# Performance work log

Hardware: AMD Instinct MI355X
Metric: run time of the kernel (lower is better)

## Reference

```python
import jax, jax.numpy as jnp
import numpy as np

U, P, D, B, H = 8192, 4096, 64, 1024, 50
EPS = 1e-8  # torch.cosine_similarity eps


def setup_inputs() -> dict:
    key = jax.random.key(0)
    ks = jax.random.split(key, 11)
    inp = {}
    for i, name in enumerate(["A_up", "A_up_NR", "A_up_FR", "A_up_TR", "A_up_UR"]):
        inp[name] = jax.random.uniform(ks[i], (U, P), jnp.float32)
    inp["user_emb"] = jax.random.normal(ks[5], (U, D), jnp.float32) * 0.1
    inp["post_emb"] = jax.random.normal(ks[6], (P, D), jnp.float32) * 0.1
    inp["user_model"] = jax.random.normal(ks[7], (U, 4), jnp.float32)
    inp["X_source_id"] = jax.random.randint(ks[8], (B,), 0, P)
    inp["X_user_id"] = jax.random.randint(ks[9], (B,), 0, U)
    inp["X_rumer_id"] = jax.random.randint(ks[10], (B, H), 0, U)
    return inp


def _forward(A, user_emb, post_emb, W, X_source_id, X_rumer_id):
    # A: [5,U,P] stacked relations [base, NR, FR, TR, UR].
    # 2-layer LightGCN-style propagation, batched across all 5 relations:
    #   u_k = A @ p_{k-1};  p_k = A^T @ u_{k-1}
    u0, p0 = user_emb, post_emb
    u1 = jnp.einsum('rup,pd->rud', A, p0)    # [5,U,D]
    p1 = jnp.einsum('rup,ud->rpd', A, u0)    # [5,P,D]
    u2 = jnp.einsum('rup,rpd->rud', A, p1)
    p2 = jnp.einsum('rup,rud->rpd', A, u1)
    # fused stack+mean over the 3 layer outputs (x0, x1, x2)
    Xu = (u0[None] + u1 + u2) / 3.0          # [5,U,D]
    X_post_full = (p0 + p1[0] + p2[0]) / 3.0  # [P,D] (base relation only)

    base = Xu[0]   # [U,D]
    rel = Xu[1:]   # [4,U,D]

    # cosine similarity of base users vs each relation variant
    n0 = jnp.linalg.norm(base, axis=1)                # [U]
    nr = jnp.linalg.norm(rel, axis=2)                 # [4,U]
    sim = jnp.sum(base[None] * rel, axis=2) / jnp.maximum(n0[None] * nr, EPS)
    sim = sim.T                                       # [U,4]
    mask = (sim == sim.max(axis=1, keepdims=True)).astype(sim.dtype)
    simm = mask * sim
    var = jnp.log(jnp.std(simm, axis=1, ddof=1) + 1.0)  # [U]; torch.std is unbiased

    user = jnp.transpose(rel, (1, 0, 2))                 # [U,4,D]
    user_embedding = jnp.einsum('ua,uad->ud', W, user)   # [U,D]
    # note: post_embedding = A_pu @ user_embedding is computed in the original
    # get_Userembedding but never used by forward's outputs; omitted.

    X_post = X_post_full[X_source_id]                    # [B,D]
    Xvu = base[X_rumer_id]                               # [B,H,D]
    Xv = var[X_rumer_id]                                 # [B,H]
    X_var_user = jnp.einsum('bh,bhd->bd', Xv, Xvu)       # [B,D]
    AugUser = jnp.mean(user_embedding[X_rumer_id], axis=1)  # [B,D]
    X_mean_user = jnp.mean(Xvu, axis=1)                  # [B,D]
    return X_post, X_var_user, AugUser, X_mean_user


def reference(A_up, A_up_NR, A_up_FR, A_up_TR, A_up_UR,
              user_emb, post_emb, user_model,
              X_source_id, X_user_id, X_rumer_id):
    A = jnp.stack([A_up, A_up_NR, A_up_FR, A_up_TR, A_up_UR], axis=0)
    return _forward(A, user_emb, post_emb, user_model, X_source_id, X_rumer_id)
```

## Files before the change

kernel.cpp:

```cpp
#include <hip/hip_runtime.h>
#include <hip/hip_bf16.h>
#include <math.h>

#define U_DIM 8192
#define P_DIM 4096
#define B_DIM 1024
#define H_DIM 50
#define EPSV  1e-8f

typedef __attribute__((ext_vector_type(8))) short short8;
typedef __attribute__((ext_vector_type(4))) short short4v;
typedef __attribute__((ext_vector_type(2))) short short2v;
typedef __attribute__((ext_vector_type(4))) float f32x4;

#define AROW(m) ((m) * 40 + ((m) & ~7))

struct APtrs { const float* p[5]; };

__device__ inline unsigned short f2bf(float f) {
    unsigned int u = __float_as_uint(f);
    u += 0x7FFFu + ((u >> 16) & 1u);
    return (unsigned short)(u >> 16);
}

template<bool TRANS>
__global__ __launch_bounds__(256, 4) void gemm_n64(
    APtrs Aps, const float* Bmat, float* C,
    int K, int ldm, long strideB, long strideC, int kseg)
{
    const int tid  = threadIdx.x;
    const int wid  = tid >> 6;
    const int lane = tid & 63;
    const int m0   = blockIdx.x * 128;
    const float* Ag = Aps.p[blockIdx.y];
    const float* Bp = Bmat + (size_t)blockIdx.y * strideB;
    float*       Cp = C    + (size_t)blockIdx.y * strideC;
    const int k_begin = blockIdx.z * kseg;

    __shared__ __align__(16) unsigned short a_s[128 * 41];
    __shared__ __align__(16) unsigned short b_s[64 * 41];

    const float* ap;
    if (!TRANS) ap = Ag + (size_t)(m0 + (tid >> 1)) * K + k_begin + ((tid & 1) << 4);
    else        ap = Ag + (size_t)(k_begin + ((tid >> 5) << 2)) * ldm + m0 + ((tid & 31) << 2);
    const float* bp = Bp + ((size_t)(k_begin + ((tid >> 4) << 1)) << 6) + ((tid & 15) << 2);

    float4 ra[4], rb[2];
    if (!TRANS) {
#pragma unroll
        for (int j = 0; j < 4; ++j) ra[j] = ((const float4*)ap)[j];
    } else {
#pragma unroll
        for (int j = 0; j < 4; ++j) ra[j] = *(const float4*)(ap + (size_t)j * ldm);
    }
    rb[0] = *(const float4*)bp;
    rb[1] = *(const float4*)(bp + 64);

    f32x4 acc[2][4] = {};
    const int iters = kseg >> 5;

    for (int it = 0; it < iters; ++it) {
        if (!TRANS) {
            const int row = tid >> 1, ho = (tid & 1) << 4;
            const float* f = (const float*)ra;
            short8 w0, w1;
#pragma unroll
            for (int j = 0; j < 8; ++j) { w0[j] = (short)f2bf(f[j]); w1[j] = (short)f2bf(f[8 + j]); }
            unsigned short* d = a_s + AROW(row) + ho;
            *(short8*)d = w0;
            *(short8*)(d + 8) = w1;
        } else {
            const int bm = tid & 31, bk = tid >> 5;
            const float* f = (const float*)ra;
#pragma unroll
            for (int jm = 0; jm < 4; ++jm) {
                short4v w = { (short)f2bf(f[jm]),     (short)f2bf(f[4 + jm]),
                              (short)f2bf(f[8 + jm]), (short)f2bf(f[12 + jm]) };
                *(short4v*)(a_s + AROW((bm << 2) + jm) + (bk << 2)) = w;
            }
        }
        {
            const int bd = tid & 15, bk2 = tid >> 4;
            const float* f = (const float*)rb;
#pragma unroll
            for (int jd = 0; jd < 4; ++jd) {
                short2v w = { (short)f2bf(f[jd]), (short)f2bf(f[4 + jd]) };
                *(short2v*)(b_s + AROW((bd << 2) + jd) + (bk2 << 1)) = w;
            }
        }
        __syncthreads();

        if (it + 1 < iters) {
            if (!TRANS) {
                ap += 32;
#pragma unroll
                for (int j = 0; j < 4; ++j) ra[j] = ((const float4*)ap)[j];
            } else {
                ap += (size_t)32 * ldm;
#pragma unroll
                for (int j = 0; j < 4; ++j) ra[j] = *(const float4*)(ap + (size_t)j * ldm);
            }
            bp += 32 * 64;
            rb[0] = *(const float4*)bp;
            rb[1] = *(const float4*)(bp + 64);
        }

        const int ko   = (lane >> 4) << 3;
        const int mrow = (wid << 5) + (lane & 15);
        short8 af0 = *(const short8*)(a_s + AROW(mrow) + ko);
        short8 af1 = *(const short8*)(a_s + AROW(mrow + 16) + ko);
#pragma unroll
        for (int nt = 0; nt < 4; ++nt) {
            short8 bf = *(const short8*)(b_s + AROW((nt << 4) + (lane & 15)) + ko);
            acc[0][nt] = __builtin_amdgcn_mfma_f32_16x16x32_bf16(af0, bf, acc[0][nt], 0, 0, 0);
            acc[1][nt] = __builtin_amdgcn_mfma_f32_16x16x32_bf16(af1, bf, acc[1][nt], 0, 0, 0);
        }
        __syncthreads();
    }

    const int col   = lane & 15;
    const int rbase = (lane >> 4) << 2;
#pragma unroll
    for (int mt = 0; mt < 2; ++mt)
#pragma unroll
        for (int nt = 0; nt < 4; ++nt)
#pragma unroll
            for (int i = 0; i < 4; ++i) {
                int row = m0 + (wid << 5) + (mt << 4) + rbase + i;
                atomicAdd(&Cp[((size_t)row << 6) + (nt << 4) + col], acc[mt][nt][i]);
            }
}

__device__ inline float wsum(float v) {
#pragma unroll
    for (int off = 32; off > 0; off >>= 1) v += __shfl_xor(v, off, 64);
    return v;
}

__global__ __launch_bounds__(256) void user_stats_k(
    const float* __restrict__ u0, const float* __restrict__ u1,
    const float* __restrict__ u2, const float* __restrict__ W,
    float* __restrict__ base_o, float* __restrict__ var_o, float* __restrict__ ue_o)
{
    int u    = blockIdx.x * 4 + (threadIdx.x >> 6);
    int lane = threadIdx.x & 63;
    size_t ud = ((size_t)u << 6) + lane;

    float b0 = u0[ud];
    float xu[5];
#pragma unroll
    for (int r = 0; r < 5; ++r)
        xu[r] = (b0 + u1[(size_t)r * U_DIM * 64 + ud] + u2[(size_t)r * U_DIM * 64 + ud]) * (1.0f / 3.0f);

    float base = xu[0];
    float n0 = sqrtf(wsum(base * base));
    float sim[4];
#pragma unroll
    for (int a = 0; a < 4; ++a) {
        float d  = wsum(base * xu[a + 1]);
        float nr = sqrtf(wsum(xu[a + 1] * xu[a + 1]));
        sim[a] = d / fmaxf(n0 * nr, EPSV);
    }
    float smax = fmaxf(fmaxf(sim[0], sim[1]), fmaxf(sim[2], sim[3]));
    float ssum = 0.0f;
    float simm[4];
#pragma unroll
    for (int a = 0; a < 4; ++a) { simm[a] = (sim[a] == smax) ? sim[a] : 0.0f; ssum += simm[a]; }
    float mean = ssum * 0.25f;
    float vs = 0.0f;
#pragma unroll
    for (int a = 0; a < 4; ++a) { float t = simm[a] - mean; vs += t * t; }
    vs *= (1.0f / 3.0f);
    float var = logf(sqrtf(vs) + 1.0f);

    float ue = 0.0f;
#pragma unroll
    for (int a = 0; a < 4; ++a) ue += W[((size_t)u << 2) + a] * xu[a + 1];

    base_o[ud] = base;
    ue_o[ud]   = ue;
    if (lane == 0) var_o[u] = var;
}

__global__ __launch_bounds__(256) void gather_k(
    const float* __restrict__ p0, const float* __restrict__ p1r0, const float* __restrict__ p2,
    const float* __restrict__ base, const float* __restrict__ var, const float* __restrict__ ue,
    const int* __restrict__ src_id, const int* __restrict__ rumer, float* __restrict__ out)
{
    int b    = blockIdx.x * 4 + (threadIdx.x >> 6);
    int lane = threadIdx.x & 63;

    int sp = src_id[b];
    size_t spd = ((size_t)sp << 6) + lane;
    out[((size_t)b << 6) + lane] = (p0[spd] + p1r0[spd] + p2[spd]) * (1.0f / 3.0f);

    float xv = 0.0f, xm = 0.0f, au = 0.0f;
    for (int h = 0; h < H_DIM; ++h) {
        int uu = rumer[b * H_DIM + h];
        size_t uud = ((size_t)uu << 6) + lane;
        float bv = base[uud];
        xv += var[uu] * bv;
        xm += bv;
        au += ue[uud];
    }
    out[((size_t)(B_DIM     + b) << 6) + lane] = xv;
    out[((size_t)(2 * B_DIM + b) << 6) + lane] = au * (1.0f / H_DIM);
    out[((size_t)(3 * B_DIM + b) << 6) + lane] = xm * (1.0f / H_DIM);
}

extern "C" void kernel_launch(void* const* d_in, const int* in_sizes, int n_in,
                              void* d_out, int out_size, void* d_ws, size_t ws_size,
                              hipStream_t stream)
{
    const float* u0 = (const float*)d_in[5];
    const float* p0 = (const float*)d_in[6];
    const float* W  = (const float*)d_in[7];
    const int* src   = (const int*)d_in[8];
    const int* rumer = (const int*)d_in[10];
    float* out = (float*)d_out;

    APtrs Ap;
    for (int r = 0; r < 5; ++r) Ap.p[r] = (const float*)d_in[r];

    float* u1   = (float*)d_ws;
    float* p1   = u1 + 5l * U_DIM * 64;
    float* p2   = p1 + 5l * P_DIM * 64;
    float* u2   = p2 + (long)P_DIM * 64;
    float* base = u2 + 5l * U_DIM * 64;
    float* var  = base + (long)U_DIM * 64;
    float* ue   = var + U_DIM;

    size_t zero_bytes = (size_t)(5l * U_DIM * 64 + 5l * P_DIM * 64 + (long)P_DIM * 64 + 5l * U_DIM * 64) * sizeof(float);
    hipMemsetAsync(d_ws, 0, zero_bytes, stream);

    gemm_n64<false><<<dim3(64, 5, 4), 256, 0, stream>>>(Ap, p0, u1, P_DIM, 0, 0, (long)U_DIM * 64, 1024);
    gemm_n64<true ><<<dim3(32, 5, 8), 256, 0, stream>>>(Ap, u0, p1, U_DIM, P_DIM, 0, (long)P_DIM * 64, 1024);
    gemm_n64<false><<<dim3(64, 5, 4), 256, 0, stream>>>(Ap, p1, u2, P_DIM, 0, (long)P_DIM * 64, (long)U_DIM * 64, 1024);
    gemm_n64<true ><<<dim3(32, 1, 16), 256, 0, stream>>>(Ap, u1, p2, U_DIM, P_DIM, 0, 0, 512);

    user_stats_k<<<U_DIM / 4, 256, 0, stream>>>(u0, u1, u2, W, base, var, ue);
    gather_k<<<B_DIM / 4, 256, 0, stream>>>(p0, p1, p2, base, var, ue, src, rumer, out);
}
```

Measured before the change: 890.1 us.

## Pre-transpose dense operands to bf16 and stream GEMM fragments directly from global

Adds a transpose kernel that converts the small dense operands (p0, u0, p1, u1) into K-major bf16 buffers so each lane can load its MFMA B fragment directly. The GEMM drops LDS staging and both barriers, loads A fragments straight from global into registers with double-buffered prefetch, and converts them to bf16 in-register. The final transposed GEMM also gets a finer K split. The aim is to remove the LDS round trip and synchronisation overhead. In exchange it adds extra launches, and the transposed-A path uses scalar strided loads that may coalesce poorly.

```diff
diff --git a/kernel.cpp b/kernel.cpp
--- a/kernel.cpp
+++ b/kernel.cpp
@@ -1,5 +1,4 @@
 #include <hip/hip_runtime.h>
-#include <hip/hip_bf16.h>
 #include <math.h>
 
 #define U_DIM 8192
@@ -9,11 +8,7 @@
 #define EPSV  1e-8f
 
 typedef __attribute__((ext_vector_type(8))) short short8;
-typedef __attribute__((ext_vector_type(4))) short short4v;
-typedef __attribute__((ext_vector_type(2))) short short2v;
 typedef __attribute__((ext_vector_type(4))) float f32x4;
-
-#define AROW(m) ((m) * 40 + ((m) & ~7))
 
 struct APtrs { const float* p[5]; };
 
@@ -23,111 +18,121 @@
     return (unsigned short)(u >> 16);
 }
 
+__global__ __launch_bounds__(256) void transpose_bf16_k(
+    const float* __restrict__ in, unsigned short* __restrict__ out,
+    int K, long strideIn, long strideOut)
+{
+    __shared__ float t[64][65];
+    const int tid = threadIdx.x;
+    const int kb  = blockIdx.x * 64;
+    const float* ip = in + (size_t)blockIdx.y * strideIn + (size_t)kb * 64;
+#pragma unroll
+    for (int j = 0; j < 16; ++j) {
+        int idx = tid + j * 256;
+        t[idx >> 6][idx & 63] = ip[idx];
+    }
+    __syncthreads();
+    unsigned short* op = out + (size_t)blockIdx.y * strideOut;
+#pragma unroll
+    for (int j = 0; j < 16; ++j) {
+        int idx = tid + j * 256;
+        int d = idx >> 6, k = idx & 63;
+        op[(size_t)d * K + kb + k] = f2bf(t[k][d]);
+    }
+}
+
 template<bool TRANS>
 __global__ __launch_bounds__(256, 4) void gemm_n64(
-    APtrs Aps, const float* Bmat, float* C,
-    int K, int ldm, long strideB, long strideC, int kseg)
-{
+    APtrs Aps, const unsigned short* __restrict__ BT, float* __restrict__ C,
+    long strideBT, long strideC, int kseg)
+{
+    const int K   = TRANS ? U_DIM : P_DIM;
     const int tid  = threadIdx.x;
     const int wid  = tid >> 6;
     const int lane = tid & 63;
-    const int m0   = blockIdx.x * 128;
+    const int l15  = lane & 15;
+    const int kg   = (lane >> 4) << 3;
+    const int m0   = blockIdx.x * 128 + wid * 32;
     const float* Ag = Aps.p[blockIdx.y];
-    const float* Bp = Bmat + (size_t)blockIdx.y * strideB;
-    float*       Cp = C    + (size_t)blockIdx.y * strideC;
-    const int k_begin = blockIdx.z * kseg;
-
-    __shared__ __align__(16) unsigned short a_s[128 * 41];
-    __shared__ __align__(16) unsigned short b_s[64 * 41];
-
-    const float* ap;
-    if (!TRANS) ap = Ag + (size_t)(m0 + (tid >> 1)) * K + k_begin + ((tid & 1) << 4);
-    else        ap = Ag + (size_t)(k_begin + ((tid >> 5) << 2)) * ldm + m0 + ((tid & 31) << 2);
-    const float* bp = Bp + ((size_t)(k_begin + ((tid >> 4) << 1)) << 6) + ((tid & 15) << 2);
-
-    float4 ra[4], rb[2];
-    if (!TRANS) {
-#pragma unroll
-        for (int j = 0; j < 4; ++j) ra[j] = ((const float4*)ap)[j];
-    } else {
-#pragma unroll
-        for (int j = 0; j < 4; ++j) ra[j] = *(const float4*)(ap + (size_t)j * ldm);
-    }
-    rb[0] = *(const float4*)bp;
-    rb[1] = *(const float4*)(bp + 64);
+    const unsigned short* Bp = BT + (size_t)blockIdx.y * strideBT;
+    float* Cp = C + (size_t)blockIdx.y * strideC;
+    const long k0 = (long)blockIdx.z * kseg + kg;
+
+    const float* a0;
+    if (!TRANS) a0 = Ag + (size_t)(m0 + l15) * K + k0;
+    else        a0 = Ag + (size_t)k0 * P_DIM + m0 + l15;
+    const unsigned short* b0 = Bp + (size_t)l15 * K + k0;
+
+    const size_t a16 = (size_t)16 * K;
+    const size_t K16 = (size_t)16 * K;
 
     f32x4 acc[2][4] = {};
-    const int iters = kseg >> 5;
-
-    for (int it = 0; it < iters; ++it) {
-        if (!TRANS) {
-            const int row = tid >> 1, ho = (tid & 1) << 4;
-            const float* f = (const float*)ra;
-            short8 w0, w1;
-#pragma unroll
-            for (int j = 0; j < 8; ++j) { w0[j] = (short)f2bf(f[j]); w1[j] = (short)f2bf(f[8 + j]); }
-            unsigned short* d = a_s + AROW(row) + ho;
-            *(short8*)d = w0;
-            *(short8*)(d + 8) = w1;
-        } else {
-            const int bm = tid & 31, bk = tid >> 5;
-            const float* f = (const float*)ra;
-#pragma unroll
-            for (int jm = 0; jm < 4; ++jm) {
-                short4v w = { (short)f2bf(f[jm]),     (short)f2bf(f[4 + jm]),
-                              (short)f2bf(f[8 + jm]), (short)f2bf(f[12 + jm]) };
-                *(short4v*)(a_s + AROW((bm << 2) + jm) + (bk << 2)) = w;
-            }
-        }
-        {
-            const int bd = tid & 15, bk2 = tid >> 4;
-            const float* f = (const float*)rb;
-#pragma unroll
-            for (int jd = 0; jd < 4; ++jd) {
-                short2v w = { (short)f2bf(f[jd]), (short)f2bf(f[4 + jd]) };
-                *(short2v*)(b_s + AROW((bd << 2) + jd) + (bk2 << 1)) = w;
-            }
-        }
-        __syncthreads();
-
-        if (it + 1 < iters) {
-            if (!TRANS) {
-                ap += 32;
-#pragma unroll
-                for (int j = 0; j < 4; ++j) ra[j] = ((const float4*)ap)[j];
-            } else {
-                ap += (size_t)32 * ldm;
-#pragma unroll
-                for (int j = 0; j < 4; ++j) ra[j] = *(const float4*)(ap + (size_t)j * ldm);
-            }
-            bp += 32 * 64;
-            rb[0] = *(const float4*)bp;
-            rb[1] = *(const float4*)(bp + 64);
-        }
-
-        const int ko   = (lane >> 4) << 3;
-        const int mrow = (wid << 5) + (lane & 15);
-        short8 af0 = *(const short8*)(a_s + AROW(mrow) + ko);
-        short8 af1 = *(const short8*)(a_s + AROW(mrow + 16) + ko);
-#pragma unroll
-        for (int nt = 0; nt < 4; ++nt) {
-            short8 bf = *(const short8*)(b_s + AROW((nt << 4) + (lane & 15)) + ko);
-            acc[0][nt] = __builtin_amdgcn_mfma_f32_16x16x32_bf16(af0, bf, acc[0][nt], 0, 0, 0);
-            acc[1][nt] = __builtin_amdgcn_mfma_f32_16x16x32_bf16(af1, bf, acc[1][nt], 0, 0, 0);
-        }
-        __syncthreads();
-    }
-
-    const int col   = lane & 15;
-    const int rbase = (lane >> 4) << 2;
+
+#define LOADA(A_, kk_) do {                                                     \
+    if (!TRANS) {                                                               \
+        const float* ap_ = a0 + (kk_);                                          \
+        A_[0] = *(const float4*)ap_;          A_[1] = *(const float4*)(ap_ + 4);\
+        A_[2] = *(const float4*)(ap_ + a16);  A_[3] = *(const float4*)(ap_ + a16 + 4); \
+    } else {                                                                    \
+        const float* ap_ = a0 + (size_t)(kk_) * P_DIM;                          \
+        A_[0].x = ap_[0 * (size_t)P_DIM];      A_[0].y = ap_[1 * (size_t)P_DIM];\
+        A_[0].z = ap_[2 * (size_t)P_DIM];      A_[0].w = ap_[3 * (size_t)P_DIM];\
+        A_[1].x = ap_[4 * (size_t)P_DIM];      A_[1].y = ap_[5 * (size_t)P_DIM];\
+        A_[1].z = ap_[6 * (size_t)P_DIM];      A_[1].w = ap_[7 * (size_t)P_DIM];\
+        A_[2].x = ap_[0 * (size_t)P_DIM + 16]; A_[2].y = ap_[1 * (size_t)P_DIM + 16]; \
+        A_[2].z = ap_[2 * (size_t)P_DIM + 16]; A_[2].w = ap_[3 * (size_t)P_DIM + 16]; \
+        A_[3].x = ap_[4 * (size_t)P_DIM + 16]; A_[3].y = ap_[5 * (size_t)P_DIM + 16]; \
+        A_[3].z = ap_[6 * (size_t)P_DIM + 16]; A_[3].w = ap_[7 * (size_t)P_DIM + 16]; \
+    }                                                                           \
+} while (0)
+
+#define LOADB(B_, kk_) do {                                                     \
+    B_[0] = *(const short8*)(b0 + (kk_));                                       \
+    B_[1] = *(const short8*)(b0 + K16 + (kk_));                                 \
+    B_[2] = *(const short8*)(b0 + 2 * K16 + (kk_));                             \
+    B_[3] = *(const short8*)(b0 + 3 * K16 + (kk_));                             \
+} while (0)
+
+#define STEP(A_, B_) do {                                                       \
+    short8 a0f, a1f;                                                            \
+    a0f[0] = (short)f2bf(A_[0].x); a0f[1] = (short)f2bf(A_[0].y);               \
+    a0f[2] = (short)f2bf(A_[0].z); a0f[3] = (short)f2bf(A_[0].w);               \
+    a0f[4] = (short)f2bf(A_[1].x); a0f[5] = (short)f2bf(A_[1].y);               \
+    a0f[6] = (short)f2bf(A_[1].z); a0f[7] = (short)f2bf(A_[1].w);               \
+    a1f[0] = (short)f2bf(A_[2].x); a1f[1] = (short)f2bf(A_[2].y);               \
+    a1f[2] = (short)f2bf(A_[2].z); a1f[3] = (short)f2bf(A_[2].w);               \
+    a1f[4] = (short)f2bf(A_[3].x); a1f[5] = (short)f2bf(A_[3].y);               \
+    a1f[6] = (short)f2bf(A_[3].z); a1f[7] = (short)f2bf(A_[3].w);               \
+    _Pragma("unroll")                                                           \
+    for (int nt = 0; nt < 4; ++nt) {                                            \
+        acc[0][nt] = __builtin_amdgcn_mfma_f32_16x16x32_bf16(a0f, B_[nt], acc[0][nt], 0, 0, 0); \
+        acc[1][nt] = __builtin_amdgcn_mfma_f32_16x16x32_bf16(a1f, B_[nt], acc[1][nt], 0, 0, 0); \
+    }                                                                           \
+} while (0)
+
+    float4 Aa[4], Ab[4];
+    short8 Ba[4], Bb[4];
+    LOADA(Aa, 0); LOADB(Ba, 0);
+    for (int kk = 0; kk < kseg; kk += 64) {
+        LOADA(Ab, kk + 32); LOADB(Bb, kk + 32);
+        STEP(Aa, Ba);
+        if (kk + 64 < kseg) { LOADA(Aa, kk + 64); LOADB(Ba, kk + 64); }
+        STEP(Ab, Bb);
+    }
+
+#undef LOADA
+#undef LOADB
+#undef STEP
+
+    const int rb4 = (lane >> 4) << 2;
 #pragma unroll
     for (int mt = 0; mt < 2; ++mt)
 #pragma unroll
         for (int nt = 0; nt < 4; ++nt)
 #pragma unroll
             for (int i = 0; i < 4; ++i) {
-                int row = m0 + (wid << 5) + (mt << 4) + rbase + i;
-                atomicAdd(&Cp[((size_t)row << 6) + (nt << 4) + col], acc[mt][nt][i]);
+                int row = m0 + (mt << 4) + rb4 + i;
+                atomicAdd(&Cp[((size_t)row << 6) + (nt << 4) + l15], acc[mt][nt][i]);
             }
 }
 
@@ -230,13 +235,25 @@
     float* var  = base + (long)U_DIM * 64;
     float* ue   = var + U_DIM;
 
+    unsigned short* p0T = (unsigned short*)base;
+    unsigned short* u0T = p0T + 64l * P_DIM;
+    unsigned short* p1T = (unsigned short*)base;
+    unsigned short* u1T = p1T + 5l * 64 * P_DIM;
+
     size_t zero_bytes = (size_t)(5l * U_DIM * 64 + 5l * P_DIM * 64 + (long)P_DIM * 64 + 5l * U_DIM * 64) * sizeof(float);
     hipMemsetAsync(d_ws, 0, zero_bytes, stream);
 
-    gemm_n64<false><<<dim3(64, 5, 4), 256, 0, stream>>>(Ap, p0, u1, P_DIM, 0, 0, (long)U_DIM * 64, 1024);
-    gemm_n64<true ><<<dim3(32, 5, 8), 256, 0, stream>>>(Ap, u0, p1, U_DIM, P_DIM, 0, (long)P_DIM * 64, 1024);
-    gemm_n64<false><<<dim3(64, 5, 4), 256, 0, stream>>>(Ap, p1, u2, P_DIM, 0, (long)P_DIM * 64, (long)U_DIM * 64, 1024);
-    gemm_n64<true ><<<dim3(32, 1, 16), 256, 0, stream>>>(Ap, u1, p2, U_DIM, P_DIM, 0, 0, 512);
+    transpose_bf16_k<<<dim3(P_DIM / 64, 1), 256, 0, stream>>>(p0, p0T, P_DIM, 0, 0);
+    transpose_bf16_k<<<dim3(U_DIM / 64, 1), 256, 0, stream>>>(u0, u0T, U_DIM, 0, 0);
+
+    gemm_n64<false><<<dim3(64, 5, 4), 256, 0, stream>>>(Ap, p0T, u1, 0, (long)U_DIM * 64, 1024);
+    gemm_n64<true ><<<dim3(32, 5, 8), 256, 0, stream>>>(Ap, u0T, p1, 0, (long)P_DIM * 64, 1024);
+
+    transpose_bf16_k<<<dim3(P_DIM / 64, 5), 256, 0, stream>>>(p1, p1T, P_DIM, (long)P_DIM * 64, 64l * P_DIM);
+    transpose_bf16_k<<<dim3(U_DIM / 64, 1), 256, 0, stream>>>(u1, u1T, U_DIM, 0, 0);
+
+    gemm_n64<false><<<dim3(64, 5, 4), 256, 0, stream>>>(Ap, p1T, u2, 64l * P_DIM, (long)U_DIM * 64, 1024);
+    gemm_n64<true ><<<dim3(32, 1, 32), 256, 0, stream>>>(Ap, u1T, p2, 0, 0, 256);
 
     user_stats_k<<<U_DIM / 4, 256, 0, stream>>>(u0, u1, u2, W, base, var, ue);
     gather_k<<<B_DIM / 4, 256, 0, stream>>>(p0, p1, p2, base, var, ue, src, rumer, out);
```

New measurement: 1.006 ms. 1.13x slower.
